# Performance work log

Measured on AMD Instinct MI355X. Metric: run time of the kernel, lower is better.

The kernel has to match this reference:

```python
import jax, jax.numpy as jnp
import numpy as np

N_NODES = 100000
N_EDGES = 1600000
IN_FEATS = 64
OUT_FEATS = 64
EDGE_FEATS = 1


def setup_inputs() -> dict:
    key = jax.random.key(0)
    ks = jax.random.split(key, 6)
    h = jax.random.normal(ks[0], (N_NODES, IN_FEATS), dtype=jnp.float32)
    e = jax.random.normal(ks[1], (N_EDGES, EDGE_FEATS), dtype=jnp.float32)
    src = jax.random.randint(ks[2], (N_EDGES,), 0, N_NODES, dtype=jnp.int32)
    dst = jax.random.randint(ks[3], (N_EDGES,), 0, N_NODES, dtype=jnp.int32)
    cat_dim = 2 * IN_FEATS + EDGE_FEATS  # 129
    W1 = jax.random.normal(ks[4], (cat_dim, OUT_FEATS), dtype=jnp.float32) / np.sqrt(cat_dim)
    b1 = jnp.zeros((OUT_FEATS,), dtype=jnp.float32)
    W2 = jax.random.normal(ks[5], (OUT_FEATS, OUT_FEATS), dtype=jnp.float32) / np.sqrt(OUT_FEATS)
    b2 = jnp.zeros((OUT_FEATS,), dtype=jnp.float32)
    return {"h": h, "e": e, "src": src, "dst": dst, "W1": W1, "b1": b1, "W2": W2, "b2": b2}


def reference(h, e, src, dst, W1, b1, W2, b2):
    # Gather per-edge features: [src_h | dst_h | e] -> (E, 2*in+edge_dim)
    x = jnp.concatenate([h[src], h[dst], e], axis=1)
    # Two-layer MLP on edges
    m = jax.nn.relu(x @ W1 + b1) @ W2 + b2  # (E, out_feats)
    # Scatter-sum messages to destination nodes
    h_new = jax.ops.segment_sum(m, dst, num_segments=h.shape[0])  # (N, out_feats)
    return h_new
```

## Files before the change

kernel.cpp:

```cpp
#include <hip/hip_runtime.h>
#include <hip/hip_bf16.h>


#define NSH 8
#define PRE_NPB 128

typedef unsigned int u32;

__device__ __forceinline__ void gload_lds16(const float* g, float* l) {
    __builtin_amdgcn_global_load_lds(
        (const __attribute__((address_space(1))) u32*)g,
        (__attribute__((address_space(3))) u32*)l,
        16, 0, 0);
}

__global__ void count_kernel(const int* __restrict__ dst, int* __restrict__ counts,
                             int* __restrict__ rank, int n_edges) {
    int i = blockIdx.x * blockDim.x + threadIdx.x;
    if (i < n_edges) rank[i] = atomicAdd(&counts[dst[i]], 1);
}

__global__ __launch_bounds__(256) void shard_sum_kernel(const int* __restrict__ counts,
                                                        int* __restrict__ shardTotal,
                                                        int n, int shsz) {
    __shared__ int ws[4];
    const int i    = blockIdx.x * 256 + threadIdx.x;
    const int lane = threadIdx.x & 63;
    const int wv   = threadIdx.x >> 6;
    int c = (i < n) ? counts[i] : 0;
    #pragma unroll
    for (int d = 1; d < 64; d <<= 1) c += __shfl_xor(c, d, 64);
    if (lane == 0) ws[wv] = c;
    __syncthreads();
    if (threadIdx.x == 0)
        atomicAdd(&shardTotal[(blockIdx.x * 256) / shsz], ws[0] + ws[1] + ws[2] + ws[3]);
}

__global__ __launch_bounds__(256) void alloc_offs_kernel(const int* __restrict__ counts,
                                                         const int* __restrict__ shardTotal,
                                                         int* __restrict__ shard_cursor,
                                                         int* __restrict__ offs, int n, int shsz) {
    __shared__ int wsum[4];
    const int i     = blockIdx.x * 256 + threadIdx.x;
    const int lane  = threadIdx.x & 63;
    const int wv    = threadIdx.x >> 6;
    const int shard = (blockIdx.x * 256) / shsz;

    const int c = (i < n) ? counts[i] : 0;
    int incl = c;
    #pragma unroll
    for (int d = 1; d < 64; d <<= 1) {
        int v = __shfl_up(incl, d, 64);
        if (lane >= d) incl += v;
    }
    const int excl = incl - c;
    if (lane == 63) wsum[wv] = incl;
    __syncthreads();
    if (threadIdx.x == 0) {
        int base0 = 0;
        #pragma unroll
        for (int t = 0; t < NSH; ++t) if (t < shard) base0 += shardTotal[t];
        const int s0 = wsum[0], s1 = wsum[1], s2 = wsum[2], s3 = wsum[3];
        const int b = base0 + atomicAdd(&shard_cursor[shard], s0 + s1 + s2 + s3);
        wsum[0] = b; wsum[1] = b + s0; wsum[2] = b + s0 + s1; wsum[3] = b + s0 + s1 + s2;
    }
    __syncthreads();
    if (i < n) offs[i] = wsum[wv] + excl;
}

__global__ void fill_kernel(const int* __restrict__ dst, const int* __restrict__ src,
                            const float* __restrict__ e,
                            const int* __restrict__ offs, const int* __restrict__ rank,
                            int2* __restrict__ meta, int n_edges) {
    const int i = blockIdx.x * blockDim.x + threadIdx.x;
    if (i >= n_edges) return;
    const int d = dst[i];
    meta[offs[d] + rank[i]] = make_int2(src[i], __float_as_int(e[i]));
}

__global__ __launch_bounds__(256, 2) void precompute_ab_kernel(
    const float* __restrict__ h, const float* __restrict__ W1, const float* __restrict__ b1,
    unsigned short* __restrict__ abf, unsigned short* __restrict__ bsf, int n_nodes)
{
    __shared__ float hbuf[2][64 * 64];
    const int lane = threadIdx.x & 63;
    const int wv   = threadIdx.x >> 6;

    const int base = blockIdx.x * PRE_NPB;
    if (base >= n_nodes) return;
    const int nrem   = n_nodes - base;
    const int ntiles = (nrem >= PRE_NPB) ? (PRE_NPB / 64) : ((nrem + 63) >> 6);

    float wreg[128];
    #pragma unroll
    for (int k = 0; k < 128; ++k) wreg[k] = W1[(size_t)k * 64 + lane];
    #pragma unroll
    for (int k = 0; k < 128; ++k) asm("" : "+v"(wreg[k]));
    const float b1l = b1[lane];

    auto stage = [&](int buf, int node_base) {
        if (node_base + 64 <= n_nodes) {
            const float* gsrc = h + (size_t)node_base * 64;
            #pragma unroll
            for (int q = 0; q < 4; ++q) {
                const int c = wv * 4 + q;
                gload_lds16(gsrc + c * 256 + lane * 4, &hbuf[buf][c * 256]);
            }
        } else {
            #pragma unroll
            for (int q = 0; q < 4; ++q) {
                const int f4 = threadIdx.x + 256 * q;
                const long gf = (long)node_base * 16 + f4;
                float4 v = make_float4(0.f, 0.f, 0.f, 0.f);
                if (gf < (long)n_nodes * 16)
                    v = reinterpret_cast<const float4*>(h)[gf];
                reinterpret_cast<float4*>(hbuf[buf])[f4] = v;
            }
        }
    };

    auto consume = [&](int buf, int node_base) {
        for (int i = 0; i < 16; ++i) {
            const int ln = wv * 16 + i;
            const int n  = node_base + ln;
            if (n < n_nodes) {
                const float4* hr = reinterpret_cast<const float4*>(&hbuf[buf][ln * 64]);
                float4 h4[16];
                #pragma unroll
                for (int k4 = 0; k4 < 16; ++k4) h4[k4] = hr[k4];
                float av = 0.f, bv = b1l;
                #pragma unroll
                for (int k4 = 0; k4 < 16; ++k4) {
                    av = fmaf(h4[k4].x, wreg[4 * k4 + 0], av);
                    bv = fmaf(h4[k4].x, wreg[64 + 4 * k4 + 0], bv);
                    av = fmaf(h4[k4].y, wreg[4 * k4 + 1], av);
                    bv = fmaf(h4[k4].y, wreg[64 + 4 * k4 + 1], bv);
                    av = fmaf(h4[k4].z, wreg[4 * k4 + 2], av);
                    bv = fmaf(h4[k4].z, wreg[64 + 4 * k4 + 2], bv);
                    av = fmaf(h4[k4].w, wreg[4 * k4 + 3], av);
                    bv = fmaf(h4[k4].w, wreg[64 + 4 * k4 + 3], bv);
                }
                __hip_bfloat16 ab = __float2bfloat16(av);
                __hip_bfloat16 bb = __float2bfloat16(bv);
                abf[(size_t)n * 64 + lane] = *reinterpret_cast<unsigned short*>(&ab);
                bsf[(size_t)n * 64 + lane] = *reinterpret_cast<unsigned short*>(&bb);
            }
        }
    };

    stage(0, base);
    __syncthreads();
    for (int t = 0; t < ntiles; ++t) {
        if (t + 1 < ntiles) stage((t + 1) & 1, base + (t + 1) * 64);
        consume(t & 1, base + t * 64);
        __syncthreads();
    }
}

__global__ __launch_bounds__(256) void node_accum_kernel(
    const unsigned short* __restrict__ abf, const unsigned short* __restrict__ bsf,
    const float* __restrict__ W1, const float* __restrict__ W2, const float* __restrict__ b2,
    const int* __restrict__ offs, const int* __restrict__ counts,
    const int2* __restrict__ meta, float* __restrict__ out, int n_nodes)
{
    const int lane = threadIdx.x & 63;
    const int wv   = __builtin_amdgcn_readfirstlane(threadIdx.x >> 6);
    const int n    = blockIdx.x * 4 + wv;
    if (n >= n_nodes) return;

    const float basel = __uint_as_float((uint)bsf[(size_t)n * 64 + lane] << 16);
    const float w128l = W1[(size_t)128 * 64 + lane];
    float acc = 0.f;

    const int beg = offs[n];
    const int np  = counts[n];

    for (int c0 = 0; c0 < np; c0 += 64) {
        const int cn = min(np - c0, 64);

        int mx = 0, my = 0;
        if (lane < cn) {
            const int2 m = meta[beg + c0 + lane];
            mx = m.x; my = m.y;
        }

        uint x0=0,x1=0,x2=0,x3=0,x4=0,x5=0,x6=0,x7=0;

        auto ld = [&](int j, uint& x) {
            const int s = __builtin_amdgcn_readlane(mx, j);
            x = (uint)abf[(size_t)s * 64 + lane];
        };
        auto step = [&](int j, uint xr) {
            const float ev = __uint_as_float((uint)__builtin_amdgcn_readlane(my, j));
            const float xv = __uint_as_float(xr << 16);
            acc += fmaxf(fmaf(ev, w128l, basel) + xv, 0.f);
        };

        if (cn > 0) ld(0, x0);
        if (cn > 1) ld(1, x1);
        if (cn > 2) ld(2, x2);
        if (cn > 3) ld(3, x3);
        if (cn > 4) ld(4, x4);
        if (cn > 5) ld(5, x5);
        if (cn > 6) ld(6, x6);
        if (cn > 7) ld(7, x7);

        int i = 0;
        while (i + 16 <= cn) {
            step(i + 0, x0); ld(i + 8,  x0);
            step(i + 1, x1); ld(i + 9,  x1);
            step(i + 2, x2); ld(i + 10, x2);
            step(i + 3, x3); ld(i + 11, x3);
            step(i + 4, x4); ld(i + 12, x4);
            step(i + 5, x5); ld(i + 13, x5);
            step(i + 6, x6); ld(i + 14, x6);
            step(i + 7, x7); ld(i + 15, x7);
            i += 8;
        }
        const int r = cn - i;
        if (r > 0)  { step(i + 0, x0); }  if (r > 8)  { ld(i + 8,  x0); }
        if (r > 1)  { step(i + 1, x1); }  if (r > 9)  { ld(i + 9,  x1); }
        if (r > 2)  { step(i + 2, x2); }  if (r > 10) { ld(i + 10, x2); }
        if (r > 3)  { step(i + 3, x3); }  if (r > 11) { ld(i + 11, x3); }
        if (r > 4)  { step(i + 4, x4); }  if (r > 12) { ld(i + 12, x4); }
        if (r > 5)  { step(i + 5, x5); }  if (r > 13) { ld(i + 13, x5); }
        if (r > 6)  { step(i + 6, x6); }  if (r > 14) { ld(i + 14, x6); }
        if (r > 7)  { step(i + 7, x7); }
        if (r > 8)  { step(i + 8,  x0); }
        if (r > 9)  { step(i + 9,  x1); }
        if (r > 10) { step(i + 10, x2); }
        if (r > 11) { step(i + 11, x3); }
        if (r > 12) { step(i + 12, x4); }
        if (r > 13) { step(i + 13, x5); }
        if (r > 14) { step(i + 14, x6); }
    }

    float o = (float)np * b2[lane];
    #pragma unroll
    for (int j = 0; j < 64; ++j) {
        const float aj = __shfl(acc, j, 64);
        o = fmaf(aj, W2[(size_t)j * 64 + lane], o);
    }
    out[(size_t)n * 64 + lane] = o;
}

extern "C" void kernel_launch(void* const* d_in, const int* in_sizes, int n_in,
                              void* d_out, int out_size, void* d_ws, size_t ws_size,
                              hipStream_t stream) {
    const float* h  = (const float*)d_in[0];
    const float* e  = (const float*)d_in[1];
    const int* src  = (const int*)d_in[2];
    const int* dst  = (const int*)d_in[3];
    const float* W1 = (const float*)d_in[4];
    const float* b1 = (const float*)d_in[5];
    const float* W2 = (const float*)d_in[6];
    const float* b2 = (const float*)d_in[7];
    float* out = (float*)d_out;

    const int n_edges = in_sizes[2];
    const int N = in_sizes[0] / 64;

    const int shsz = ((N + NSH * 256 - 1) / (NSH * 256)) * 256;

    int* counts       = (int*)d_ws;
    int* shardTotal   = counts + N;
    int* shard_cursor = shardTotal + NSH;
    int* offs         = shard_cursor + NSH;
    int* rank         = offs + N;
    int2* meta        = (int2*)(rank + n_edges);
    unsigned short* abf = (unsigned short*)(meta + n_edges);
    unsigned short* bsf = abf + (size_t)64 * N;

    hipMemsetAsync(counts, 0, ((size_t)N + 2 * NSH) * sizeof(int), stream);

    const int eb = (n_edges + 255) / 256;
    const int nb = (N + 255) / 256;
    const int pg = (N + PRE_NPB - 1) / PRE_NPB;

    precompute_ab_kernel<<<pg, 256, 0, stream>>>(h, W1, b1, abf, bsf, N);
    count_kernel<<<eb, 256, 0, stream>>>(dst, counts, rank, n_edges);
    shard_sum_kernel<<<nb, 256, 0, stream>>>(counts, shardTotal, N, shsz);
    alloc_offs_kernel<<<nb, 256, 0, stream>>>(counts, shardTotal, shard_cursor, offs, N, shsz);
    fill_kernel<<<eb, 256, 0, stream>>>(dst, src, e, offs, rank, meta, n_edges);
    node_accum_kernel<<<(N + 3) / 4, 256, 0, stream>>>(abf, bsf, W1, W2, b2,
                                                       offs, counts, meta, out, N);
}
```

Before: 229.3 us.

## Drop shard offset pass and LDS staging in node precompute

Removes the shard_sum kernel and sharded cursors so the CSR offset allocation uses a single global atomic cursor, saving one kernel launch and a pass over counts. The precompute kernel stops double-buffering h through LDS with async global-to-LDS loads. Instead each wave handles 32 consecutive nodes and reads rows straight from global memory with float4 loads, using a register-held zero offset to shape codegen. The costs are more contention on a single atomic and per-row global loads that are broadcast across lanes rather than staged cooperatively.

```diff
diff --git a/kernel.cpp b/kernel.cpp
--- a/kernel.cpp
+++ b/kernel.cpp
@@ -2,17 +2,9 @@
 #include <hip/hip_bf16.h>
 
 
-#define NSH 8
-#define PRE_NPB 128
+#define PRE_NPW 32
 
 typedef unsigned int u32;
-
-__device__ __forceinline__ void gload_lds16(const float* g, float* l) {
-    __builtin_amdgcn_global_load_lds(
-        (const __attribute__((address_space(1))) u32*)g,
-        (__attribute__((address_space(3))) u32*)l,
-        16, 0, 0);
-}
 
 __global__ void count_kernel(const int* __restrict__ dst, int* __restrict__ counts,
                              int* __restrict__ rank, int n_edges) {
@@ -20,31 +12,13 @@
     if (i < n_edges) rank[i] = atomicAdd(&counts[dst[i]], 1);
 }
 
-__global__ __launch_bounds__(256) void shard_sum_kernel(const int* __restrict__ counts,
-                                                        int* __restrict__ shardTotal,
-                                                        int n, int shsz) {
-    __shared__ int ws[4];
+__global__ __launch_bounds__(256) void alloc_offs_kernel(const int* __restrict__ counts,
+                                                         int* __restrict__ gcursor,
+                                                         int* __restrict__ offs, int n) {
+    __shared__ int wsum[4];
     const int i    = blockIdx.x * 256 + threadIdx.x;
     const int lane = threadIdx.x & 63;
     const int wv   = threadIdx.x >> 6;
-    int c = (i < n) ? counts[i] : 0;
-    #pragma unroll
-    for (int d = 1; d < 64; d <<= 1) c += __shfl_xor(c, d, 64);
-    if (lane == 0) ws[wv] = c;
-    __syncthreads();
-    if (threadIdx.x == 0)
-        atomicAdd(&shardTotal[(blockIdx.x * 256) / shsz], ws[0] + ws[1] + ws[2] + ws[3]);
-}
-
-__global__ __launch_bounds__(256) void alloc_offs_kernel(const int* __restrict__ counts,
-                                                         const int* __restrict__ shardTotal,
-                                                         int* __restrict__ shard_cursor,
-                                                         int* __restrict__ offs, int n, int shsz) {
-    __shared__ int wsum[4];
-    const int i     = blockIdx.x * 256 + threadIdx.x;
-    const int lane  = threadIdx.x & 63;
-    const int wv    = threadIdx.x >> 6;
-    const int shard = (blockIdx.x * 256) / shsz;
 
     const int c = (i < n) ? counts[i] : 0;
     int incl = c;
@@ -57,11 +31,8 @@
     if (lane == 63) wsum[wv] = incl;
     __syncthreads();
     if (threadIdx.x == 0) {
-        int base0 = 0;
-        #pragma unroll
-        for (int t = 0; t < NSH; ++t) if (t < shard) base0 += shardTotal[t];
         const int s0 = wsum[0], s1 = wsum[1], s2 = wsum[2], s3 = wsum[3];
-        const int b = base0 + atomicAdd(&shard_cursor[shard], s0 + s1 + s2 + s3);
+        const int b = atomicAdd(gcursor, s0 + s1 + s2 + s3);
         wsum[0] = b; wsum[1] = b + s0; wsum[2] = b + s0 + s1; wsum[3] = b + s0 + s1 + s2;
     }
     __syncthreads();
@@ -82,78 +53,46 @@
     const float* __restrict__ h, const float* __restrict__ W1, const float* __restrict__ b1,
     unsigned short* __restrict__ abf, unsigned short* __restrict__ bsf, int n_nodes)
 {
-    __shared__ float hbuf[2][64 * 64];
     const int lane = threadIdx.x & 63;
     const int wv   = threadIdx.x >> 6;
-
-    const int base = blockIdx.x * PRE_NPB;
-    if (base >= n_nodes) return;
-    const int nrem   = n_nodes - base;
-    const int ntiles = (nrem >= PRE_NPB) ? (PRE_NPB / 64) : ((nrem + 63) >> 6);
+    const int n0   = (blockIdx.x * 4 + wv) * PRE_NPW;
+    if (n0 >= n_nodes) return;
+
+    int z;
+    asm volatile("v_mov_b32 %0, 0" : "=v"(z));
 
     float wreg[128];
     #pragma unroll
     for (int k = 0; k < 128; ++k) wreg[k] = W1[(size_t)k * 64 + lane];
     #pragma unroll
-    for (int k = 0; k < 128; ++k) asm("" : "+v"(wreg[k]));
+    for (int k = 0; k < 128; ++k) asm volatile("" : "+v"(wreg[k]));
     const float b1l = b1[lane];
 
-    auto stage = [&](int buf, int node_base) {
-        if (node_base + 64 <= n_nodes) {
-            const float* gsrc = h + (size_t)node_base * 64;
-            #pragma unroll
-            for (int q = 0; q < 4; ++q) {
-                const int c = wv * 4 + q;
-                gload_lds16(gsrc + c * 256 + lane * 4, &hbuf[buf][c * 256]);
-            }
-        } else {
-            #pragma unroll
-            for (int q = 0; q < 4; ++q) {
-                const int f4 = threadIdx.x + 256 * q;
-                const long gf = (long)node_base * 16 + f4;
-                float4 v = make_float4(0.f, 0.f, 0.f, 0.f);
-                if (gf < (long)n_nodes * 16)
-                    v = reinterpret_cast<const float4*>(h)[gf];
-                reinterpret_cast<float4*>(hbuf[buf])[f4] = v;
-            }
+    for (int t = 0; t < PRE_NPW; ++t) {
+        const int n = n0 + t;
+        if (n >= n_nodes) break;
+
+        const float4* hr = reinterpret_cast<const float4*>(h + (size_t)n * 64 + z);
+        float4 h4[16];
+        #pragma unroll
+        for (int k4 = 0; k4 < 16; ++k4) h4[k4] = hr[k4];
+
+        float av = 0.f, bv = b1l;
+        #pragma unroll
+        for (int k4 = 0; k4 < 16; ++k4) {
+            av = fmaf(h4[k4].x, wreg[4 * k4 + 0], av);
+            bv = fmaf(h4[k4].x, wreg[64 + 4 * k4 + 0], bv);
+            av = fmaf(h4[k4].y, wreg[4 * k4 + 1], av);
+            bv = fmaf(h4[k4].y, wreg[64 + 4 * k4 + 1], bv);
+            av = fmaf(h4[k4].z, wreg[4 * k4 + 2], av);
+            bv = fmaf(h4[k4].z, wreg[64 + 4 * k4 + 2], bv);
+            av = fmaf(h4[k4].w, wreg[4 * k4 + 3], av);
+            bv = fmaf(h4[k4].w, wreg[64 + 4 * k4 + 3], bv);
         }
-    };
-
-    auto consume = [&](int buf, int node_base) {
-        for (int i = 0; i < 16; ++i) {
-            const int ln = wv * 16 + i;
-            const int n  = node_base + ln;
-            if (n < n_nodes) {
-                const float4* hr = reinterpret_cast<const float4*>(&hbuf[buf][ln * 64]);
-                float4 h4[16];
-                #pragma unroll
-                for (int k4 = 0; k4 < 16; ++k4) h4[k4] = hr[k4];
-                float av = 0.f, bv = b1l;
-                #pragma unroll
-                for (int k4 = 0; k4 < 16; ++k4) {
-                    av = fmaf(h4[k4].x, wreg[4 * k4 + 0], av);
-                    bv = fmaf(h4[k4].x, wreg[64 + 4 * k4 + 0], bv);
-                    av = fmaf(h4[k4].y, wreg[4 * k4 + 1], av);
-                    bv = fmaf(h4[k4].y, wreg[64 + 4 * k4 + 1], bv);
-                    av = fmaf(h4[k4].z, wreg[4 * k4 + 2], av);
-                    bv = fmaf(h4[k4].z, wreg[64 + 4 * k4 + 2], bv);
-                    av = fmaf(h4[k4].w, wreg[4 * k4 + 3], av);
-                    bv = fmaf(h4[k4].w, wreg[64 + 4 * k4 + 3], bv);
-                }
-                __hip_bfloat16 ab = __float2bfloat16(av);
-                __hip_bfloat16 bb = __float2bfloat16(bv);
-                abf[(size_t)n * 64 + lane] = *reinterpret_cast<unsigned short*>(&ab);
-                bsf[(size_t)n * 64 + lane] = *reinterpret_cast<unsigned short*>(&bb);
-            }
-        }
-    };
-
-    stage(0, base);
-    __syncthreads();
-    for (int t = 0; t < ntiles; ++t) {
-        if (t + 1 < ntiles) stage((t + 1) & 1, base + (t + 1) * 64);
-        consume(t & 1, base + t * 64);
-        __syncthreads();
+        __hip_bfloat16 ab = __float2bfloat16(av);
+        __hip_bfloat16 bb = __float2bfloat16(bv);
+        abf[(size_t)n * 64 + lane] = *reinterpret_cast<unsigned short*>(&ab);
+        bsf[(size_t)n * 64 + lane] = *reinterpret_cast<unsigned short*>(&bb);
     }
 }
 
@@ -260,27 +199,23 @@
     const int n_edges = in_sizes[2];
     const int N = in_sizes[0] / 64;
 
-    const int shsz = ((N + NSH * 256 - 1) / (NSH * 256)) * 256;
-
-    int* counts       = (int*)d_ws;
-    int* shardTotal   = counts + N;
-    int* shard_cursor = shardTotal + NSH;
-    int* offs         = shard_cursor + NSH;
-    int* rank         = offs + N;
-    int2* meta        = (int2*)(rank + n_edges);
+    int* counts  = (int*)d_ws;
+    int* gcursor = counts + N;
+    int* offs    = gcursor + 8;
+    int* rank    = offs + N;
+    int2* meta   = (int2*)(rank + n_edges);
     unsigned short* abf = (unsigned short*)(meta + n_edges);
     unsigned short* bsf = abf + (size_t)64 * N;
 
-    hipMemsetAsync(counts, 0, ((size_t)N + 2 * NSH) * sizeof(int), stream);
+    hipMemsetAsync(counts, 0, ((size_t)N + 8) * sizeof(int), stream);
 
     const int eb = (n_edges + 255) / 256;
     const int nb = (N + 255) / 256;
-    const int pg = (N + PRE_NPB - 1) / PRE_NPB;
+    const int pg = (N + 4 * PRE_NPW - 1) / (4 * PRE_NPW);
 
     precompute_ab_kernel<<<pg, 256, 0, stream>>>(h, W1, b1, abf, bsf, N);
     count_kernel<<<eb, 256, 0, stream>>>(dst, counts, rank, n_edges);
-    shard_sum_kernel<<<nb, 256, 0, stream>>>(counts, shardTotal, N, shsz);
-    alloc_offs_kernel<<<nb, 256, 0, stream>>>(counts, shardTotal, shard_cursor, offs, N, shsz);
+    alloc_offs_kernel<<<nb, 256, 0, stream>>>(counts, gcursor, offs, N);
     fill_kernel<<<eb, 256, 0, stream>>>(dst, src, e, offs, rank, meta, n_edges);
     node_accum_kernel<<<(N + 3) / 4, 256, 0, stream>>>(abf, bsf, W1, W2, b2,
                                                        offs, counts, meta, out, N);
```

Measured after the change: 715.9 us. 3.12x slower.
